# Optimization experiments

Measured on AMD Instinct MI355X. Metric: run time of the kernel, lower is better.

The kernel has to match this reference:

```python
import jax, jax.numpy as jnp
import numpy as np

D_MODEL = 1024
NUM_HEADS = 16
HEAD_DIM = D_MODEL // NUM_HEADS  # 64
ROPE_THETA = 10000.0
SEQ_LEN = 4096
BATCH = 1


def apply_rope(x, positions, theta=ROPE_THETA):
    # x: [b, h, s, d], positions: [s]
    d = x.shape[-1]
    inv_freq = theta ** (-jnp.arange(0, d, 2, dtype=jnp.float32) / d)  # [d/2]
    angles = positions.astype(jnp.float32)[:, None] * inv_freq[None, :]  # [s, d/2]
    cos = jnp.cos(angles)  # [s, d/2]
    sin = jnp.sin(angles)
    x1 = x[..., 0::2]  # [b, h, s, d/2]
    x2 = x[..., 1::2]
    r1 = x1 * cos - x2 * sin
    r2 = x1 * sin + x2 * cos
    # interleave back to [..., d]
    out = jnp.stack([r1, r2], axis=-1).reshape(x.shape)
    return out.astype(x.dtype)


def setup_inputs() -> dict:
    key = jax.random.key(0)
    k_x, k_qkv, k_o = jax.random.split(key, 3)
    scale_in = 1.0 / np.sqrt(D_MODEL)
    return {
        "x": jax.random.normal(k_x, (BATCH, SEQ_LEN, D_MODEL), dtype=jnp.float32),
        "token_positions": jnp.arange(SEQ_LEN, dtype=jnp.int64 if jax.config.jax_enable_x64 else jnp.int32),
        "w_qkv": jax.random.normal(k_qkv, (3 * D_MODEL, D_MODEL), dtype=jnp.float32) * scale_in,
        "w_o": jax.random.normal(k_o, (D_MODEL, D_MODEL), dtype=jnp.float32) * scale_in,
    }


def reference(x, token_positions, w_qkv, w_o):
    b, s, _ = x.shape
    # QKV projection (Linear without bias, weight [out, in])
    x_qkv = jnp.einsum('bsd,ed->bse', x, w_qkv)  # [b, s, 3*d_model]
    # rearrange 'b s (three heads kv) -> three b heads s kv'
    x_qkv = x_qkv.reshape(b, s, 3, NUM_HEADS, HEAD_DIM)
    x_qkv = jnp.transpose(x_qkv, (2, 0, 3, 1, 4))  # [3, b, h, s, d]
    q, k, v = x_qkv[0], x_qkv[1], x_qkv[2]
    q = apply_rope(q, token_positions)
    k = apply_rope(k, token_positions)
    # scaled dot-product attention with causal mask
    scores = jnp.einsum('bhnd,bhmd->bhnm', q, k) / jnp.sqrt(jnp.float32(HEAD_DIM))
    causal = jnp.tril(jnp.ones((s, s), dtype=bool))  # [s, s]
    scores = jnp.where(causal[None, None], scores, jnp.float32(-jnp.inf))
    weights = jax.nn.softmax(scores, axis=-1)
    attn = jnp.einsum('bhnm,bhmd->bhnd', weights, v)  # [b, h, s, d]
    attn = jnp.transpose(attn, (0, 2, 1, 3)).reshape(b, s, NUM_HEADS * HEAD_DIM)
    return jnp.einsum('bsd,ed->bse', attn, w_o)
```

## Files before the change

### kernel.cpp

```cpp
#include <hip/hip_runtime.h>

#define SEQ 4096
#define DMODEL 1024
#define HEADS 16
#define HD 64
#define NQKV 3072

typedef __attribute__((ext_vector_type(8))) __bf16 bf16x8;
typedef __attribute__((ext_vector_type(4))) __bf16 bf16x4;
typedef __attribute__((ext_vector_type(8))) short short8;
typedef __attribute__((ext_vector_type(4))) float f32x4;

__device__ __forceinline__ unsigned short f2bf(float f) {
    unsigned u = __builtin_bit_cast(unsigned, f);
    return (unsigned short)((u + 0x7fffu + ((u >> 16) & 1u)) >> 16);
}
__device__ __forceinline__ float bf2f(unsigned short h) {
    return __builtin_bit_cast(float, (unsigned)h << 16);
}

__device__ __forceinline__ void gload16(const void* g, void* l) {
    __builtin_amdgcn_global_load_lds(
        (const __attribute__((address_space(1))) unsigned int*)g,
        (__attribute__((address_space(3))) unsigned int*)l, 16, 0, 0);
}

__global__ void f2bf_all(const float* __restrict__ x, const float* __restrict__ wqkv,
                         const float* __restrict__ wo, unsigned short* __restrict__ dst) {
    const int N0 = SEQ * DMODEL / 4;
    const int N1 = N0 + NQKV * DMODEL / 4;
    const int NT = N1 + DMODEL * DMODEL / 4;
    int i = blockIdx.x * 256 + threadIdx.x;
    int stride = gridDim.x * 256;
    for (; i < NT; i += stride) {
        const float4* src;
        if (i < N0)      src = reinterpret_cast<const float4*>(x) + i;
        else if (i < N1) src = reinterpret_cast<const float4*>(wqkv) + (i - N0);
        else             src = reinterpret_cast<const float4*>(wo) + (i - N1);
        float4 f = *src;
        ushort4 o;
        o.x = f2bf(f.x); o.y = f2bf(f.y); o.z = f2bf(f.z); o.w = f2bf(f.w);
        reinterpret_cast<ushort4*>(dst)[i] = o;
    }
}

template <int EPI>
__global__ __launch_bounds__(256) void gemm_bt(const unsigned short* __restrict__ A,
                                               const unsigned short* __restrict__ B,
                                               float* __restrict__ outF,
                                               unsigned short* __restrict__ outB,
                                               int M, int N, int K) {
    alignas(16) __shared__ unsigned short a_lds[2][128 * 32];
    alignas(16) __shared__ unsigned short b_lds[2][128 * 32];
    const int tid = threadIdx.x;
    const int wave = tid >> 6, lane = tid & 63;
    const int l16 = lane & 15, g = lane >> 4;
    const int wr = wave >> 1, wc = wave & 1;
    const int bm = blockIdx.x, bn = blockIdx.y;

    const int lrow = lane >> 2;
    const int lcol = (lane & 3) * 8;

    const unsigned short* Ag = A + (size_t)(bm * 128 + lrow) * K + lcol;
    const unsigned short* Bg = B + (size_t)(bn * 128 + lrow) * K + lcol;

    f32x4 acc[4][4] = {};
    const int NS = K / 32;

    auto STAGE = [&](int b, int ks) {
#pragma unroll
        for (int j = 0; j < 2; ++j) {
            int chunk = wave * 2 + j;
            gload16(Ag + (size_t)(chunk * 16) * K + ks * 32, a_lds[b] + chunk * 512);
            gload16(Bg + (size_t)(chunk * 16) * K + ks * 32, b_lds[b] + chunk * 512);
        }
    };

    STAGE(0, 0);

    for (int ks = 0; ks < NS; ++ks) {
        const int cur = ks & 1;
        asm volatile("s_waitcnt vmcnt(0)" ::: "memory");
        __builtin_amdgcn_s_barrier();
        if (ks + 1 < NS) STAGE(cur ^ 1, ks + 1);

        bf16x8 af[4], bfr[4];
#pragma unroll
        for (int m = 0; m < 4; ++m)
            af[m] = *reinterpret_cast<const bf16x8*>(a_lds[cur] + (wr * 64 + m * 16 + l16) * 32 + g * 8);
#pragma unroll
        for (int n = 0; n < 4; ++n)
            bfr[n] = *reinterpret_cast<const bf16x8*>(b_lds[cur] + (wc * 64 + n * 16 + l16) * 32 + g * 8);
        __builtin_amdgcn_s_setprio(1);
#pragma unroll
        for (int m = 0; m < 4; ++m)
#pragma unroll
            for (int n = 0; n < 4; ++n)
                acc[m][n] = __builtin_amdgcn_mfma_f32_16x16x32_bf16(af[m], bfr[n], acc[m][n], 0, 0, 0);
        __builtin_amdgcn_s_setprio(0);
    }

#pragma unroll
    for (int m = 0; m < 4; ++m)
#pragma unroll
        for (int n = 0; n < 4; ++n)
#pragma unroll
            for (int r = 0; r < 4; ++r) {
                int row = bm * 128 + wr * 64 + m * 16 + g * 4 + r;
                int col = bn * 128 + wc * 64 + n * 16 + l16;
                float v = acc[m][n][r];
                if (EPI == 0) {
                    int part = col >> 10;
                    int hd = col & 1023;
                    int h = hd >> 6, d = hd & 63;
                    outB[(size_t)((part * HEADS + h) * SEQ + row) * HD + d] = f2bf(v);
                } else {
                    outF[(size_t)row * N + col] = v;
                }
            }
}

__global__ __launch_bounds__(256) void rope_kernel(unsigned short* qkv, const int* __restrict__ pos) {
    int idx = blockIdx.x * 256 + threadIdx.x;
    int chunk = idx & 7;
    int row = idx >> 3;
    int s = row & (SEQ - 1);
    int ph = row >> 12;
    float p = (float)pos[s];
    float scale = (ph < HEADS) ? 0.125f * 1.4426950408889634f : 1.0f;
    unsigned short* base = qkv + ((size_t)ph * SEQ + s) * HD + chunk * 8;
    short8 v = *reinterpret_cast<short8*>(base);
    short8 o;
    const float k = -13.287712379549449f / 32.0f;
#pragma unroll
    for (int j = 0; j < 4; ++j) {
        int i = chunk * 4 + j;
        float ang = p * exp2f((float)i * k);
        float sn, cs;
        sincosf(ang, &sn, &cs);
        float x1 = bf2f((unsigned short)v[2 * j]);
        float x2 = bf2f((unsigned short)v[2 * j + 1]);
        o[2 * j]     = (short)f2bf((x1 * cs - x2 * sn) * scale);
        o[2 * j + 1] = (short)f2bf((x1 * sn + x2 * cs) * scale);
    }
    *reinterpret_cast<short8*>(base) = o;
}

__global__ __launch_bounds__(256) void transpose_v(const unsigned short* __restrict__ qkv,
                                                   unsigned short* __restrict__ vt) {
    const int st = blockIdx.x;
    const int h = blockIdx.y;
    __shared__ unsigned short tile[64][72];
    const unsigned short* Vg = qkv + (size_t)((2 * HEADS + h) * SEQ) * HD;
    const int tid = threadIdx.x;
#pragma unroll
    for (int j = 0; j < 2; ++j) {
        int b = (tid + j * 256) * 8;
        int row = b >> 6;
        int col = b & 63;
        short8 v = *reinterpret_cast<const short8*>(Vg + (size_t)(st * 64 + row) * HD + col);
#pragma unroll
        for (int i = 0; i < 8; ++i) tile[row][col + i] = (unsigned short)v[i];
    }
    __syncthreads();
#pragma unroll
    for (int j = 0; j < 2; ++j) {
        int b = (tid + j * 256) * 8;
        int d = b >> 6;
        int sc = b & 63;
        short8 o;
#pragma unroll
        for (int i = 0; i < 8; ++i) o[i] = (short)tile[sc + i][d];
        *reinterpret_cast<short8*>(vt + (size_t)(h * HD + d) * SEQ + st * 64 + sc) = o;
    }
}

__global__ __launch_bounds__(512) void attn_kernel(const unsigned short* __restrict__ qkv,
                                                   const unsigned short* __restrict__ vt,
                                                   unsigned short* __restrict__ attnout) {
    const int bid = blockIdx.x;
    const int xcd = bid & 7;
    const int slt = bid >> 3;
    const int j = slt & 31, hlf = slt >> 5;
    const int h = xcd * 2 + (j & 1);
    const int qb = hlf ? (j >> 1) : (31 - (j >> 1));

    const int tid = threadIdx.x;
    const int wave = tid >> 6, lane = tid & 63;
    const int l16 = lane & 15, g = lane >> 4;

    alignas(16) __shared__ unsigned short k_lds[2][128 * 64];
    alignas(16) __shared__ unsigned short v_lds[2][64 * 128];
    alignas(16) __shared__ unsigned short p_lds[8][16 * 64];

    const unsigned short* Qg = qkv + (size_t)((0 * HEADS + h) * SEQ) * HD;
    const unsigned short* Kg = qkv + (size_t)((1 * HEADS + h) * SEQ) * HD;
    const unsigned short* VTg = vt + (size_t)h * HD * SEQ;

    const int qbase = qb * 128 + wave * 16;
    bf16x8 qf[2];
    qf[0] = *reinterpret_cast<const bf16x8*>(Qg + (size_t)(qbase + l16) * HD + g * 8);
    qf[1] = *reinterpret_cast<const bf16x8*>(Qg + (size_t)(qbase + l16) * HD + 32 + g * 8);

    bf16x8 ones;
#pragma unroll
    for (int j2 = 0; j2 < 8; ++j2) ones[j2] = (__bf16)1.0f;

    f32x4 o_acc[4] = {};
    f32x4 l_acc = {};
    float m_r = -1e30f;

    char* pwave = (char*)p_lds + wave * 2048;
    const int rsw = (l16 & 7) << 4;

    auto STAGE = [&](int b, int kt) {
#pragma unroll
        for (int i = 0; i < 2; ++i) {
            int base = wave * 2048 + i * 1024;
            int byte = base + lane * 16;
            int krow = byte >> 7;
            int kc8 = ((byte >> 4) & 7) ^ (krow & 7);
            gload16(Kg + (size_t)(kt * 128 + krow) * HD + kc8 * 8, (char*)k_lds[b] + base);
            int vrow = byte >> 8;
            int vc16 = ((byte >> 4) & 15) ^ (vrow & 7);
            gload16(VTg + (size_t)vrow * SEQ + kt * 128 + vc16 * 8, (char*)v_lds[b] + base);
        }
    };

    STAGE(0, 0);

    for (int kt = 0; kt <= qb; ++kt) {
        const int cur = kt & 1;
        asm volatile("s_waitcnt vmcnt(0)" ::: "memory");
        __builtin_amdgcn_s_barrier();
        if (kt < qb) STAGE(cur ^ 1, kt + 1);

        const bool doB = (kt * 128 + 64) <= (qbase + 15);

        f32x4 s[8] = {};
        __builtin_amdgcn_s_setprio(1);
#pragma unroll
        for (int nt = 0; nt < 4; ++nt) {
            int row = nt * 16 + l16;
#pragma unroll
            for (int kk = 0; kk < 2; ++kk) {
                bf16x8 kf = *reinterpret_cast<const bf16x8*>(
                    (char*)k_lds[cur] + row * 128 + (((kk * 4 + g) << 4) ^ rsw));
                s[nt] = __builtin_amdgcn_mfma_f32_16x16x32_bf16(kf, qf[kk], s[nt], 0, 0, 0);
            }
        }
        if (doB) {
#pragma unroll
            for (int nt = 0; nt < 4; ++nt) {
                int row = 64 + nt * 16 + l16;
#pragma unroll
                for (int kk = 0; kk < 2; ++kk) {
                    bf16x8 kf = *reinterpret_cast<const bf16x8*>(
                        (char*)k_lds[cur] + row * 128 + (((kk * 4 + g) << 4) ^ rsw));
                    s[4 + nt] = __builtin_amdgcn_mfma_f32_16x16x32_bf16(kf, qf[kk], s[4 + nt], 0, 0, 0);
                }
            }
        }
        __builtin_amdgcn_s_setprio(0);

        if (kt * 128 + 127 > qbase) {
            int qrow = qbase + l16;
#pragma unroll
            for (int nt = 0; nt < 4; ++nt)
#pragma unroll
                for (int r = 0; r < 4; ++r) {
                    int kv = kt * 128 + nt * 16 + g * 4 + r;
                    if (kv > qrow) s[nt][r] = -1e30f;
                    if (kv + 64 > qrow) s[4 + nt][r] = -1e30f;
                }
        }

        f32x4 m4;
#pragma unroll
        for (int r = 0; r < 4; ++r) {
            float a = fmaxf(fmaxf(s[0][r], s[1][r]), fmaxf(s[2][r], s[3][r]));
            float b = fmaxf(fmaxf(s[4][r], s[5][r]), fmaxf(s[6][r], s[7][r]));
            m4[r] = fmaxf(a, b);
        }
        float mx = fmaxf(fmaxf(m4[0], m4[1]), fmaxf(m4[2], m4[3]));
        mx = fmaxf(mx, __shfl_xor(mx, 16));
        mx = fmaxf(mx, __shfl_xor(mx, 32));

        if (__any(mx > m_r + 8.0f)) {
            float mnew = fmaxf(m_r, mx);
            float alpha = __builtin_amdgcn_exp2f(m_r - mnew);
            m_r = mnew;
#pragma unroll
            for (int dt = 0; dt < 4; ++dt)
#pragma unroll
                for (int r = 0; r < 4; ++r) o_acc[dt][r] *= alpha;
            l_acc[0] *= alpha;
        }

#pragma unroll
        for (int i = 0; i < 8; ++i)
#pragma unroll
            for (int r = 0; r < 4; ++r) s[i][r] = __builtin_amdgcn_exp2f(s[i][r] - m_r);

        __builtin_amdgcn_s_setprio(1);
#pragma unroll
        for (int h64 = 0; h64 < 2; ++h64) {
            if (h64 && !doB) break;
#pragma unroll
            for (int nt = 0; nt < 4; ++nt) {
                bf16x4 pb;
#pragma unroll
                for (int r = 0; r < 4; ++r) pb[r] = (__bf16)s[h64 * 4 + nt][r];
                *reinterpret_cast<bf16x4*>(pwave + l16 * 128 + ((nt * 32 + g * 8) ^ rsw)) = pb;
            }
            bf16x8 pfrag[2];
#pragma unroll
            for (int kk = 0; kk < 2; ++kk)
                pfrag[kk] = *reinterpret_cast<const bf16x8*>(
                    pwave + l16 * 128 + (((kk * 4 + g) << 4) ^ rsw));

#pragma unroll
            for (int dt = 0; dt < 4; ++dt) {
                int row = dt * 16 + l16;
#pragma unroll
                for (int kk = 0; kk < 2; ++kk) {
                    bf16x8 vf = *reinterpret_cast<const bf16x8*>(
                        (char*)v_lds[cur] + row * 256 + ((h64 * 128 + kk * 64 + g * 16) ^ rsw));
                    o_acc[dt] = __builtin_amdgcn_mfma_f32_16x16x32_bf16(vf, pfrag[kk], o_acc[dt], 0, 0, 0);
                }
            }
            l_acc = __builtin_amdgcn_mfma_f32_16x16x32_bf16(ones, pfrag[0], l_acc, 0, 0, 0);
            l_acc = __builtin_amdgcn_mfma_f32_16x16x32_bf16(ones, pfrag[1], l_acc, 0, 0, 0);
        }
        __builtin_amdgcn_s_setprio(0);
    }

    float inv = 1.0f / l_acc[0];
    int q = qbase + l16;
#pragma unroll
    for (int dt = 0; dt < 4; ++dt) {
        ushort4 ov;
        ov.x = f2bf(o_acc[dt][0] * inv);
        ov.y = f2bf(o_acc[dt][1] * inv);
        ov.z = f2bf(o_acc[dt][2] * inv);
        ov.w = f2bf(o_acc[dt][3] * inv);
        *reinterpret_cast<ushort4*>(attnout + (size_t)q * DMODEL + h * HD + dt * 16 + g * 4) = ov;
    }
}

extern "C" void kernel_launch(void* const* d_in, const int* in_sizes, int n_in,
                              void* d_out, int out_size, void* d_ws, size_t ws_size,
                              hipStream_t stream) {
    const float* x = (const float*)d_in[0];
    const int* pos = (const int*)d_in[1];
    const float* wqkv = (const float*)d_in[2];
    const float* wo = (const float*)d_in[3];
    float* out = (float*)d_out;

    unsigned short* xb = (unsigned short*)d_ws;
    unsigned short* wqkvb = xb + (size_t)SEQ * DMODEL;
    unsigned short* wob = wqkvb + (size_t)NQKV * DMODEL;
    unsigned short* qkvp = wob + (size_t)DMODEL * DMODEL;
    unsigned short* vt = qkvp + (size_t)3 * HEADS * SEQ * HD;
    unsigned short* attnb = vt + (size_t)HEADS * HD * SEQ;

    f2bf_all<<<2048, 256, 0, stream>>>(x, wqkv, wo, xb);

    dim3 g1(SEQ / 128, NQKV / 128);
    gemm_bt<0><<<g1, 256, 0, stream>>>(xb, wqkvb, nullptr, qkvp, SEQ, NQKV, DMODEL);

    rope_kernel<<<(2 * HEADS * SEQ * 8) / 256, 256, 0, stream>>>(qkvp, pos);
    transpose_v<<<dim3(SEQ / 64, HEADS), 256, 0, stream>>>(qkvp, vt);
    attn_kernel<<<512, 512, 0, stream>>>(qkvp, vt, attnb);

    dim3 g2(SEQ / 128, DMODEL / 128);
    gemm_bt<1><<<g2, 256, 0, stream>>>(attnb, wob, out, nullptr, SEQ, DMODEL, DMODEL);
}
```

Measured before the change: 149.3 us.

## Give each attention wave 32 query rows and triple-buffer GEMM loads

```diff
diff --git a/kernel.cpp b/kernel.cpp
--- a/kernel.cpp
+++ b/kernel.cpp
@@ -50,8 +50,8 @@
                                                float* __restrict__ outF,
                                                unsigned short* __restrict__ outB,
                                                int M, int N, int K) {
-    alignas(16) __shared__ unsigned short a_lds[2][128 * 32];
-    alignas(16) __shared__ unsigned short b_lds[2][128 * 32];
+    alignas(16) __shared__ unsigned short a_lds[3][128 * 32];
+    alignas(16) __shared__ unsigned short b_lds[3][128 * 32];
     const int tid = threadIdx.x;
     const int wave = tid >> 6, lane = tid & 63;
     const int l16 = lane & 15, g = lane >> 4;
@@ -77,12 +77,14 @@
     };
 
     STAGE(0, 0);
+    STAGE(1, 1);
 
     for (int ks = 0; ks < NS; ++ks) {
-        const int cur = ks & 1;
-        asm volatile("s_waitcnt vmcnt(0)" ::: "memory");
+        const int cur = ks % 3;
+        if (ks + 1 < NS) asm volatile("s_waitcnt vmcnt(4)" ::: "memory");
+        else             asm volatile("s_waitcnt vmcnt(0)" ::: "memory");
         __builtin_amdgcn_s_barrier();
-        if (ks + 1 < NS) STAGE(cur ^ 1, ks + 1);
+        if (ks + 2 < NS) STAGE((ks + 2) % 3, ks + 2);
 
         bf16x8 af[4], bfr[4];
 #pragma unroll
@@ -175,7 +177,7 @@
     }
 }
 
-__global__ __launch_bounds__(512) void attn_kernel(const unsigned short* __restrict__ qkv,
+__global__ __launch_bounds__(256) void attn_kernel(const unsigned short* __restrict__ qkv,
                                                    const unsigned short* __restrict__ vt,
                                                    unsigned short* __restrict__ attnout) {
     const int bid = blockIdx.x;
@@ -191,32 +193,37 @@
 
     alignas(16) __shared__ unsigned short k_lds[2][128 * 64];
     alignas(16) __shared__ unsigned short v_lds[2][64 * 128];
-    alignas(16) __shared__ unsigned short p_lds[8][16 * 64];
+    alignas(16) __shared__ unsigned short p_lds[4][32 * 64];
 
     const unsigned short* Qg = qkv + (size_t)((0 * HEADS + h) * SEQ) * HD;
     const unsigned short* Kg = qkv + (size_t)((1 * HEADS + h) * SEQ) * HD;
     const unsigned short* VTg = vt + (size_t)h * HD * SEQ;
 
-    const int qbase = qb * 128 + wave * 16;
-    bf16x8 qf[2];
-    qf[0] = *reinterpret_cast<const bf16x8*>(Qg + (size_t)(qbase + l16) * HD + g * 8);
-    qf[1] = *reinterpret_cast<const bf16x8*>(Qg + (size_t)(qbase + l16) * HD + 32 + g * 8);
+    const int qbase = qb * 128 + wave * 32;
+
+    bf16x8 qf[2][2];
+#pragma unroll
+    for (int f = 0; f < 2; ++f)
+#pragma unroll
+        for (int kk = 0; kk < 2; ++kk)
+            qf[f][kk] = *reinterpret_cast<const bf16x8*>(
+                Qg + (size_t)(qbase + f * 16 + l16) * HD + kk * 32 + g * 8);
 
     bf16x8 ones;
 #pragma unroll
     for (int j2 = 0; j2 < 8; ++j2) ones[j2] = (__bf16)1.0f;
 
-    f32x4 o_acc[4] = {};
-    f32x4 l_acc = {};
-    float m_r = -1e30f;
-
-    char* pwave = (char*)p_lds + wave * 2048;
+    f32x4 o_acc[2][4] = {};
+    f32x4 l_acc[2] = {};
+    float m_r[2] = {-1e30f, -1e30f};
+
+    char* pwave = (char*)p_lds + wave * 4096;
     const int rsw = (l16 & 7) << 4;
 
     auto STAGE = [&](int b, int kt) {
 #pragma unroll
-        for (int i = 0; i < 2; ++i) {
-            int base = wave * 2048 + i * 1024;
+        for (int i = 0; i < 4; ++i) {
+            int base = wave * 4096 + i * 1024;
             int byte = base + lane * 16;
             int krow = byte >> 7;
             int kc8 = ((byte >> 4) & 7) ^ (krow & 7);
@@ -235,9 +242,9 @@
         __builtin_amdgcn_s_barrier();
         if (kt < qb) STAGE(cur ^ 1, kt + 1);
 
-        const bool doB = (kt * 128 + 64) <= (qbase + 15);
-
-        f32x4 s[8] = {};
+        const bool doB = (kt * 128 + 64) <= (qbase + 31);
+
+        f32x4 s[2][8] = {};
         __builtin_amdgcn_s_setprio(1);
 #pragma unroll
         for (int nt = 0; nt < 4; ++nt) {
@@ -246,7 +253,8 @@
             for (int kk = 0; kk < 2; ++kk) {
                 bf16x8 kf = *reinterpret_cast<const bf16x8*>(
                     (char*)k_lds[cur] + row * 128 + (((kk * 4 + g) << 4) ^ rsw));
-                s[nt] = __builtin_amdgcn_mfma_f32_16x16x32_bf16(kf, qf[kk], s[nt], 0, 0, 0);
+                s[0][nt] = __builtin_amdgcn_mfma_f32_16x16x32_bf16(kf, qf[0][kk], s[0][nt], 0, 0, 0);
+                s[1][nt] = __builtin_amdgcn_mfma_f32_16x16x32_bf16(kf, qf[1][kk], s[1][nt], 0, 0, 0);
             }
         }
         if (doB) {
@@ -257,67 +265,87 @@
                 for (int kk = 0; kk < 2; ++kk) {
                     bf16x8 kf = *reinterpret_cast<const bf16x8*>(
                         (char*)k_lds[cur] + row * 128 + (((kk * 4 + g) << 4) ^ rsw));
-                    s[4 + nt] = __builtin_amdgcn_mfma_f32_16x16x32_bf16(kf, qf[kk], s[4 + nt], 0, 0, 0);
+                    s[0][4 + nt] = __builtin_amdgcn_mfma_f32_16x16x32_bf16(kf, qf[0][kk], s[0][4 + nt], 0, 0, 0);
+                    s[1][4 + nt] = __builtin_amdgcn_mfma_f32_16x16x32_bf16(kf, qf[1][kk], s[1][4 + nt], 0, 0, 0);
                 }
             }
         }
         __builtin_amdgcn_s_setprio(0);
 
-        if (kt * 128 + 127 > qbase) {
-            int qrow = qbase + l16;
+        if (kt == qb) {
+#pragma unroll
+            for (int f = 0; f < 2; ++f) {
+                int qrow = qbase + f * 16 + l16;
+#pragma unroll
+                for (int nt = 0; nt < 4; ++nt)
+#pragma unroll
+                    for (int r = 0; r < 4; ++r) {
+                        int kv = kt * 128 + nt * 16 + g * 4 + r;
+                        if (kv > qrow) s[f][nt][r] = -1e30f;
+                        if (kv + 64 > qrow) s[f][4 + nt][r] = -1e30f;
+                    }
+            }
+        }
+
+#pragma unroll
+        for (int f = 0; f < 2; ++f) {
+            float a0 = fmaxf(fmaxf(s[f][0][0], s[f][0][1]), fmaxf(s[f][0][2], s[f][0][3]));
+            float a1 = fmaxf(fmaxf(s[f][1][0], s[f][1][1]), fmaxf(s[f][1][2], s[f][1][3]));
+            float a2 = fmaxf(fmaxf(s[f][2][0], s[f][2][1]), fmaxf(s[f][2][2], s[f][2][3]));
+            float a3 = fmaxf(fmaxf(s[f][3][0], s[f][3][1]), fmaxf(s[f][3][2], s[f][3][3]));
+            float mx = fmaxf(fmaxf(a0, a1), fmaxf(a2, a3));
+            if (doB) {
+                float b0 = fmaxf(fmaxf(s[f][4][0], s[f][4][1]), fmaxf(s[f][4][2], s[f][4][3]));
+                float b1 = fmaxf(fmaxf(s[f][5][0], s[f][5][1]), fmaxf(s[f][5][2], s[f][5][3]));
+                float b2 = fmaxf(fmaxf(s[f][6][0], s[f][6][1]), fmaxf(s[f][6][2], s[f][6][3]));
+                float b3 = fmaxf(fmaxf(s[f][7][0], s[f][7][1]), fmaxf(s[f][7][2], s[f][7][3]));
+                mx = fmaxf(mx, fmaxf(fmaxf(b0, b1), fmaxf(b2, b3)));
+            }
+            mx = fmaxf(mx, __shfl_xor(mx, 16));
+            mx = fmaxf(mx, __shfl_xor(mx, 32));
+
+            if (__any(mx > m_r[f] + 8.0f)) {
+                float mnew = fmaxf(m_r[f], mx);
+                float alpha = __builtin_amdgcn_exp2f(m_r[f] - mnew);
+                m_r[f] = mnew;
+#pragma unroll
+                for (int dt = 0; dt < 4; ++dt)
+#pragma unroll
+                    for (int r = 0; r < 4; ++r) o_acc[f][dt][r] *= alpha;
+                l_acc[f][0] *= alpha;
+            }
 #pragma unroll
             for (int nt = 0; nt < 4; ++nt)
 #pragma unroll
-                for (int r = 0; r < 4; ++r) {
-                    int kv = kt * 128 + nt * 16 + g * 4 + r;
-                    if (kv > qrow) s[nt][r] = -1e30f;
-                    if (kv + 64 > qrow) s[4 + nt][r] = -1e30f;
-                }
-        }
-
-        f32x4 m4;
-#pragma unroll
-        for (int r = 0; r < 4; ++r) {
-            float a = fmaxf(fmaxf(s[0][r], s[1][r]), fmaxf(s[2][r], s[3][r]));
-            float b = fmaxf(fmaxf(s[4][r], s[5][r]), fmaxf(s[6][r], s[7][r]));
-            m4[r] = fmaxf(a, b);
-        }
-        float mx = fmaxf(fmaxf(m4[0], m4[1]), fmaxf(m4[2], m4[3]));
-        mx = fmaxf(mx, __shfl_xor(mx, 16));
-        mx = fmaxf(mx, __shfl_xor(mx, 32));
-
-        if (__any(mx > m_r + 8.0f)) {
-            float mnew = fmaxf(m_r, mx);
-            float alpha = __builtin_amdgcn_exp2f(m_r - mnew);
-            m_r = mnew;
-#pragma unroll
-            for (int dt = 0; dt < 4; ++dt)
-#pragma unroll
-                for (int r = 0; r < 4; ++r) o_acc[dt][r] *= alpha;
-            l_acc[0] *= alpha;
-        }
-
-#pragma unroll
-        for (int i = 0; i < 8; ++i)
-#pragma unroll
-            for (int r = 0; r < 4; ++r) s[i][r] = __builtin_amdgcn_exp2f(s[i][r] - m_r);
+                for (int r = 0; r < 4; ++r) s[f][nt][r] = __builtin_amdgcn_exp2f(s[f][nt][r] - m_r[f]);
+            if (doB) {
+#pragma unroll
+                for (int nt = 4; nt < 8; ++nt)
+#pragma unroll
+                    for (int r = 0; r < 4; ++r) s[f][nt][r] = __builtin_amdgcn_exp2f(s[f][nt][r] - m_r[f]);
+            }
+        }
 
         __builtin_amdgcn_s_setprio(1);
 #pragma unroll
         for (int h64 = 0; h64 < 2; ++h64) {
             if (h64 && !doB) break;
 #pragma unroll
-            for (int nt = 0; nt < 4; ++nt) {
-                bf16x4 pb;
-#pragma unroll
-                for (int r = 0; r < 4; ++r) pb[r] = (__bf16)s[h64 * 4 + nt][r];
-                *reinterpret_cast<bf16x4*>(pwave + l16 * 128 + ((nt * 32 + g * 8) ^ rsw)) = pb;
-            }
-            bf16x8 pfrag[2];
-#pragma unroll
-            for (int kk = 0; kk < 2; ++kk)
-                pfrag[kk] = *reinterpret_cast<const bf16x8*>(
-                    pwave + l16 * 128 + (((kk * 4 + g) << 4) ^ rsw));
+            for (int f = 0; f < 2; ++f)
+#pragma unroll
+                for (int nt = 0; nt < 4; ++nt) {
+                    bf16x4 pb;
+#pragma unroll
+                    for (int r = 0; r < 4; ++r) pb[r] = (__bf16)s[f][h64 * 4 + nt][r];
+                    *reinterpret_cast<bf16x4*>(pwave + (f * 16 + l16) * 128 + ((nt * 32 + g * 8) ^ rsw)) = pb;
+                }
+            bf16x8 pfrag[2][2];
+#pragma unroll
+            for (int f = 0; f < 2; ++f)
+#pragma unroll
+                for (int kk = 0; kk < 2; ++kk)
+                    pfrag[f][kk] = *reinterpret_cast<const bf16x8*>(
+                        pwave + (f * 16 + l16) * 128 + (((kk * 4 + g) << 4) ^ rsw));
 
 #pragma unroll
             for (int dt = 0; dt < 4; ++dt) {
@@ -326,25 +354,32 @@
                 for (int kk = 0; kk < 2; ++kk) {
                     bf16x8 vf = *reinterpret_cast<const bf16x8*>(
                         (char*)v_lds[cur] + row * 256 + ((h64 * 128 + kk * 64 + g * 16) ^ rsw));
-                    o_acc[dt] = __builtin_amdgcn_mfma_f32_16x16x32_bf16(vf, pfrag[kk], o_acc[dt], 0, 0, 0);
+                    o_acc[0][dt] = __builtin_amdgcn_mfma_f32_16x16x32_bf16(vf, pfrag[0][kk], o_acc[0][dt], 0, 0, 0);
+                    o_acc[1][dt] = __builtin_amdgcn_mfma_f32_16x16x32_bf16(vf, pfrag[1][kk], o_acc[1][dt], 0, 0, 0);
                 }
             }
-            l_acc = __builtin_amdgcn_mfma_f32_16x16x32_bf16(ones, pfrag[0], l_acc, 0, 0, 0);
-            l_acc = __builtin_amdgcn_mfma_f32_16x16x32_bf16(ones, pfrag[1], l_acc, 0, 0, 0);
+#pragma unroll
+            for (int f = 0; f < 2; ++f) {
+                l_acc[f] = __builtin_amdgcn_mfma_f32_16x16x32_bf16(ones, pfrag[f][0], l_acc[f], 0, 0, 0);
+                l_acc[f] = __builtin_amdgcn_mfma_f32_16x16x32_bf16(ones, pfrag[f][1], l_acc[f], 0, 0, 0);
+            }
         }
         __builtin_amdgcn_s_setprio(0);
     }
 
-    float inv = 1.0f / l_acc[0];
-    int q = qbase + l16;
-#pragma unroll
-    for (int dt = 0; dt < 4; ++dt) {
-        ushort4 ov;
-        ov.x = f2bf(o_acc[dt][0] * inv);
-        ov.y = f2bf(o_acc[dt][1] * inv);
-        ov.z = f2bf(o_acc[dt][2] * inv);
-        ov.w = f2bf(o_acc[dt][3] * inv);
-        *reinterpret_cast<ushort4*>(attnout + (size_t)q * DMODEL + h * HD + dt * 16 + g * 4) = ov;
+#pragma unroll
+    for (int f = 0; f < 2; ++f) {
+        float inv = 1.0f / l_acc[f][0];
+        int q = qbase + f * 16 + l16;
+#pragma unroll
+        for (int dt = 0; dt < 4; ++dt) {
+            ushort4 ov;
+            ov.x = f2bf(o_acc[f][dt][0] * inv);
+            ov.y = f2bf(o_acc[f][dt][1] * inv);
+            ov.z = f2bf(o_acc[f][dt][2] * inv);
+            ov.w = f2bf(o_acc[f][dt][3] * inv);
+            *reinterpret_cast<ushort4*>(attnout + (size_t)q * DMODEL + h * HD + dt * 16 + g * 4) = ov;
+        }
     }
 }
 
@@ -371,7 +406,7 @@
 
     rope_kernel<<<(2 * HEADS * SEQ * 8) / 256, 256, 0, stream>>>(qkvp, pos);
     transpose_v<<<dim3(SEQ / 64, HEADS), 256, 0, stream>>>(qkvp, vt);
-    attn_kernel<<<512, 512, 0, stream>>>(qkvp, vt, attnb);
+    attn_kernel<<<512, 256, 0, stream>>>(qkvp, vt, attnb);
 
     dim3 g2(SEQ / 128, DMODEL / 128);
     gemm_bt<1><<<g2, 256, 0, stream>>>(attnb, wob, out, nullptr, SEQ, DMODEL, DMODEL);
```

New measurement: 197.1 us. +32.0%, slower.
